# Kernel optimization log

Measured on AMD Instinct MI355X. Metric: run time of the kernel, lower is better.

The kernel has to match this reference:

```python
import jax, jax.numpy as jnp
import numpy as np

N_NODES = 50000
EPS = 1e-16


def seg_softmax(att, seg, n):
    # att: [E, H], softmax over edges sharing the same destination (seg)
    m = jax.ops.segment_max(att, seg, num_segments=n)
    m = jnp.where(jnp.isfinite(m), m, 0.0)
    e = jnp.exp(att - m[seg])
    s = jax.ops.segment_sum(e, seg, num_segments=n)
    return e / (s[seg] + EPS)


def gat_layer(x, W, b, a_l, a_r, row, col, n, nhead, out_feats, alpha, act):
    h = (x @ W).reshape(-1, nhead, out_feats)           # [N, H, F]
    h = jnp.nan_to_num(h)
    h_l = jnp.sum(a_l * h, axis=-1)                     # [N, H]
    h_r = jnp.sum(a_r * h, axis=-1)                     # [N, H]
    e = h_l[row] + h_r[col]                             # [E, H]
    e = jax.nn.leaky_relu(e, negative_slope=alpha)
    att = seg_softmax(e, row, n)                        # softmax per destination node
    # sparse multi-head aggregation: out[i] = sum_{e: row[e]=i} att[e] * h[col[e]]
    msg = att[:, :, None] * h[col]                      # [E, H, F]
    out = jax.ops.segment_sum(msg, row, num_segments=n) # [N, H, F]
    out = out.reshape(n, nhead * out_feats) + b
    if act:
        out = jax.nn.relu(out)
    return out


def setup_inputs() -> dict:
    key = jax.random.key(0)
    ks = jax.random.split(key, 10)
    N, E = N_NODES, 800000
    x = jax.random.normal(ks[0], (N, 256), dtype=jnp.float32)
    row = jax.random.randint(ks[1], (E,), 0, N)
    col = jax.random.randint(ks[2], (E,), 0, N)
    g = 1.414  # xavier-like scale handled via normal * small std
    W1 = jax.random.normal(ks[3], (256, 128), dtype=jnp.float32) * (g / np.sqrt(256 + 128))
    b1 = jnp.zeros((128,), dtype=jnp.float32)
    al1 = jax.random.normal(ks[4], (1, 4, 32), dtype=jnp.float32) * 0.1
    ar1 = jax.random.normal(ks[5], (1, 4, 32), dtype=jnp.float32) * 0.1
    W2 = jax.random.normal(ks[6], (128, 64), dtype=jnp.float32) * (g / np.sqrt(128 + 64))
    b2 = jnp.zeros((64,), dtype=jnp.float32)
    al2 = jax.random.normal(ks[7], (1, 1, 64), dtype=jnp.float32) * 0.1
    ar2 = jax.random.normal(ks[8], (1, 1, 64), dtype=jnp.float32) * 0.1
    return {"x": x, "row": row, "col": col, "W1": W1, "b1": b1, "al1": al1,
            "ar1": ar1, "W2": W2, "b2": b2, "al2": al2, "ar2": ar2}


def reference(x, row, col, W1, b1, al1, ar1, W2, b2, al2, ar2):
    n = N_NODES
    h = gat_layer(x, W1, b1, al1, ar1, row, col, n, nhead=4, out_feats=32, alpha=0.2, act=True)
    out = gat_layer(h, W2, b2, al2, ar2, row, col, n, nhead=1, out_feats=64, alpha=0.2, act=False)
    return out
```

## Files before the change

kernel.cpp:

```cpp
#include <hip/hip_runtime.h>
#include <hip/hip_bf16.h>
#include <hip/hip_fp16.h>
#include <math.h>

#define ALPHA 0.2f
#define LOG2E 1.44269504088896f
#define CAP 8192

typedef _Float16 half8 __attribute__((ext_vector_type(8)));
typedef float f32x4 __attribute__((ext_vector_type(4)));

__global__ __launch_bounds__(256) void setup_kernel(
    int* __restrict__ gcursor,
    const float* __restrict__ W1, _Float16* __restrict__ W1t,
    const float* __restrict__ W2, _Float16* __restrict__ W2t) {
    const int blk = blockIdx.x, tid = threadIdx.x;
    if (blk == 0) {
        gcursor[tid] = 0;
    } else if (blk <= 128) {
        int i = (blk - 1) * 256 + tid;
        int k = i >> 7, c = i & 127;
        W1t[c * 256 + k] = (_Float16)W1[i];
    } else {
        int j = (blk - 129) * 256 + tid;
        int k = j >> 6, c = j & 63;
        W2t[c * 128 + k] = (_Float16)W2[j];
    }
}

__global__ __launch_bounds__(256) void part_kernel(const int* __restrict__ row,
                                                   const int* __restrict__ col,
                                                   int* __restrict__ gcursor,
                                                   unsigned* __restrict__ tmp, int E) {
    __shared__ int h[256];
    __shared__ int rsv[256];
    const int tid = threadIdx.x;
    const int base = blockIdx.x * 4096;
    h[tid] = 0;
    __syncthreads();
#pragma unroll
    for (int k = 0; k < 16; ++k) {
        int i = base + k * 256 + tid;
        if (i < E) atomicAdd(&h[row[i] >> 8], 1);
    }
    __syncthreads();
    if (h[tid]) rsv[tid] = atomicAdd(&gcursor[tid], h[tid]);
    __syncthreads();
    h[tid] = 0;
    __syncthreads();
#pragma unroll
    for (int k = 0; k < 16; ++k) {
        int i = base + k * 256 + tid;
        if (i < E) {
            int r = row[i];
            int b = r >> 8;
            int loc = atomicAdd(&h[b], 1);
            tmp[(size_t)b * CAP + rsv[b] + loc] = ((unsigned)r << 16) | (unsigned)col[i];
        }
    }
}

__global__ __launch_bounds__(256) void bucket_kernel(const unsigned* __restrict__ tmp,
                                                     const int* __restrict__ gcursor,
                                                     unsigned* __restrict__ startcnt,
                                                     unsigned short* __restrict__ csr_col,
                                                     int N) {
    __shared__ int h[256];
    __shared__ int rs[256];
    __shared__ int wtot[4];
    const int k = blockIdx.x, tid = threadIdx.x;
    const int lane = tid & 63, wid = tid >> 6;
    const int base = k * CAP;
    const int count = gcursor[k];
    h[tid] = 0;
    __syncthreads();
    for (int p = tid; p < count; p += 256) atomicAdd(&h[(tmp[base + p] >> 16) & 255], 1);
    __syncthreads();
    int v = h[tid];
    int sc = v;
#pragma unroll
    for (int d = 1; d < 64; d <<= 1) {
        int u = __shfl_up(sc, d);
        if (lane >= d) sc += u;
    }
    if (lane == 63) wtot[wid] = sc;
    __syncthreads();
    int add = 0;
    for (int w = 0; w < wid; ++w) add += wtot[w];
    rs[tid] = sc - v + add + base;
    __syncthreads();
    int gr = k * 256 + tid;
    if (gr < N) startcnt[gr] = ((unsigned)rs[tid] << 11) | (unsigned)v;
    h[tid] = 0;
    __syncthreads();
    for (int p = tid; p < count; p += 256) {
        unsigned t = tmp[base + p];
        int rl = (t >> 16) & 255;
        int loc = atomicAdd(&h[rl], 1);
        csr_col[rs[rl] + loc] = (unsigned short)(t & 0xFFFF);
    }
}

__global__ __launch_bounds__(256) void gemm1_mfma(
    const float* __restrict__ x, const _Float16* __restrict__ Wt,
    const float* __restrict__ al, const float* __restrict__ ar,
    _Float16* __restrict__ h, float* __restrict__ hl, float* __restrict__ hr, int N)
{
    __shared__ _Float16 xs[32 * 256];
    const int tid = threadIdx.x;
    const int lane = tid & 63, wc = tid >> 6;
    const int row0 = blockIdx.x * 32;
    const int col0 = wc * 32;

#pragma unroll
    for (int it = 0; it < 8; ++it) {
        int i = it * 256 + tid;
        int r = i >> 6, c4 = i & 63;
        int gr = row0 + r;
        float4 v = {0.f, 0.f, 0.f, 0.f};
        if (gr < N) v = *(const float4*)(x + (size_t)gr * 256 + c4 * 4);
        union { _Float16 p[4]; uint2 u; } pk;
        pk.p[0] = (_Float16)v.x; pk.p[1] = (_Float16)v.y;
        pk.p[2] = (_Float16)v.z; pk.p[3] = (_Float16)v.w;
        int byte = r * 512 + c4 * 8;
        byte ^= (r & 7) << 4;
        *reinterpret_cast<uint2*>(reinterpret_cast<char*>(xs) + byte) = pk.u;
    }

    const _Float16* wbase = Wt + (size_t)(col0 + (lane & 15)) * 256 + (lane >> 4) * 8;

    __syncthreads();

    f32x4 acc[2][2] = {};
    half8 bf0[2], bf1[2], af0[2], af1[2];

    auto loadB = [&](int s, half8* dst) {
        dst[0] = *(const half8*)(wbase + s * 32);
        dst[1] = *(const half8*)(wbase + 16 * 256 + s * 32);
    };
    auto loadA = [&](int s, half8* dst) {
#pragma unroll
        for (int m = 0; m < 2; ++m) {
            int r = m * 16 + (lane & 15);
            int byte = r * 512 + s * 64 + (lane >> 4) * 16;
            byte ^= (r & 7) << 4;
            dst[m] = *reinterpret_cast<const half8*>(
                reinterpret_cast<const char*>(xs) + byte);
        }
    };
    auto domfma = [&](half8* a, half8* bvec) {
#pragma unroll
        for (int m = 0; m < 2; ++m)
#pragma unroll
            for (int n = 0; n < 2; ++n)
                acc[m][n] = __builtin_amdgcn_mfma_f32_16x16x32_f16(
                    a[m], bvec[n], acc[m][n], 0, 0, 0);
    };

    loadB(0, bf0); loadA(0, af0);
#pragma unroll
    for (int s = 0; s < 8; s += 2) {
        if (s + 1 < 8) { loadB(s + 1, bf1); loadA(s + 1, af1); }
        domfma(af0, bf0);
        if (s + 2 < 8) { loadB(s + 2, bf0); loadA(s + 2, af0); }
        if (s + 1 < 8) domfma(af1, bf1);
    }

#pragma unroll
    for (int m = 0; m < 2; ++m) {
        int grow_base = row0 + m * 16 + (lane >> 4) * 4;
#pragma unroll
        for (int n = 0; n < 2; ++n) {
            int gcol = col0 + n * 16 + (lane & 15);
#pragma unroll
            for (int reg = 0; reg < 4; ++reg) {
                int grow = grow_base + reg;
                if (grow < N) h[(size_t)grow * 128 + gcol] = (_Float16)acc[m][n][reg];
            }
        }
    }

    const float al0 = al[col0 + (lane & 15)],      ar0 = ar[col0 + (lane & 15)];
    const float al1 = al[col0 + 16 + (lane & 15)], ar1 = ar[col0 + 16 + (lane & 15)];
#pragma unroll
    for (int m = 0; m < 2; ++m) {
#pragma unroll
        for (int reg = 0; reg < 4; ++reg) {
            float l = al0 * acc[m][0][reg] + al1 * acc[m][1][reg];
            float r = ar0 * acc[m][0][reg] + ar1 * acc[m][1][reg];
#pragma unroll
            for (int msk = 1; msk < 16; msk <<= 1) {
                l += __shfl_xor(l, msk);
                r += __shfl_xor(r, msk);
            }
            int grow = row0 + m * 16 + (lane >> 4) * 4 + reg;
            if ((lane & 15) == 0 && grow < N) {
                hl[grow * 4 + wc] = l * LOG2E;
                hr[grow * 4 + wc] = r * LOG2E;
            }
        }
    }
}

__global__ __launch_bounds__(256) void gemm2_mfma(
    const _Float16* __restrict__ xin, const _Float16* __restrict__ Wt,
    const float* __restrict__ al, const float* __restrict__ ar,
    _Float16* __restrict__ h, float* __restrict__ hl, float* __restrict__ hr, int N)
{
    __shared__ _Float16 xs[32 * 128];
    __shared__ float plds[32][4], prds[32][4];
    const int tid = threadIdx.x;
    const int lane = tid & 63, wc = tid >> 6;
    const int row0 = blockIdx.x * 32;
    const int col0 = wc * 16;

#pragma unroll
    for (int it = 0; it < 2; ++it) {
        int i = it * 256 + tid;
        int r = i >> 4, c16 = i & 15;
        int gr = row0 + r;
        uint4 v = {0, 0, 0, 0};
        if (gr < N) v = *(const uint4*)(xin + (size_t)gr * 128 + c16 * 8);
        int byte = r * 256 + c16 * 16;
        byte ^= (r & 7) << 4;
        *reinterpret_cast<uint4*>(reinterpret_cast<char*>(xs) + byte) = v;
    }

    const _Float16* wbase = Wt + (size_t)(col0 + (lane & 15)) * 128 + (lane >> 4) * 8;

    __syncthreads();

    f32x4 acc[2] = {};
    half8 bf0, bf1, af0[2], af1[2];

    auto loadA = [&](int s, half8* dst) {
#pragma unroll
        for (int m = 0; m < 2; ++m) {
            int r = m * 16 + (lane & 15);
            int byte = r * 256 + s * 64 + (lane >> 4) * 16;
            byte ^= (r & 7) << 4;
            dst[m] = *reinterpret_cast<const half8*>(
                reinterpret_cast<const char*>(xs) + byte);
        }
    };

    bf0 = *(const half8*)(wbase); loadA(0, af0);
#pragma unroll
    for (int s = 0; s < 4; s += 2) {
        if (s + 1 < 4) { bf1 = *(const half8*)(wbase + (s + 1) * 32); loadA(s + 1, af1); }
#pragma unroll
        for (int m = 0; m < 2; ++m)
            acc[m] = __builtin_amdgcn_mfma_f32_16x16x32_f16(af0[m], bf0, acc[m], 0, 0, 0);
        if (s + 2 < 4) { bf0 = *(const half8*)(wbase + (s + 2) * 32); loadA(s + 2, af0); }
        if (s + 1 < 4)
#pragma unroll
            for (int m = 0; m < 2; ++m)
                acc[m] = __builtin_amdgcn_mfma_f32_16x16x32_f16(af1[m], bf1, acc[m], 0, 0, 0);
    }

#pragma unroll
    for (int m = 0; m < 2; ++m) {
        int grow_base = row0 + m * 16 + (lane >> 4) * 4;
        int gcol = col0 + (lane & 15);
#pragma unroll
        for (int reg = 0; reg < 4; ++reg) {
            int grow = grow_base + reg;
            if (grow < N) h[(size_t)grow * 64 + gcol] = (_Float16)acc[m][reg];
        }
    }

    const float alv = al[col0 + (lane & 15)], arv = ar[col0 + (lane & 15)];
#pragma unroll
    for (int m = 0; m < 2; ++m) {
#pragma unroll
        for (int reg = 0; reg < 4; ++reg) {
            float l = alv * acc[m][reg];
            float r = arv * acc[m][reg];
#pragma unroll
            for (int msk = 1; msk < 16; msk <<= 1) {
                l += __shfl_xor(l, msk);
                r += __shfl_xor(r, msk);
            }
            int ri = m * 16 + (lane >> 4) * 4 + reg;
            if ((lane & 15) == 0) { plds[ri][wc] = l; prds[ri][wc] = r; }
        }
    }
    __syncthreads();
    if (tid < 32) {
        int grow = row0 + tid;
        if (grow < N) {
            float l = plds[tid][0] + plds[tid][1] + plds[tid][2] + plds[tid][3];
            float r = prds[tid][0] + prds[tid][1] + prds[tid][2] + prds[tid][3];
            hl[grow] = l * LOG2E;
            hr[grow] = r * LOG2E;
        }
    }
}

__global__ __launch_bounds__(256) void agg1_kernel(
    const unsigned* __restrict__ startcnt, const unsigned short* __restrict__ csr_col,
    const float* __restrict__ hls, const float* __restrict__ hrs,
    const _Float16* __restrict__ h, const float* __restrict__ b,
    _Float16* __restrict__ out, int N)
{
    const int i = blockIdx.x * 4 + (threadIdx.x >> 6);
    if (i >= N) return;
    const int lane = threadIdx.x & 63;
    const int q = lane >> 4;
    const int fl = lane & 15;
    const int head = fl >> 2;
    const unsigned pk = startcnt[i];
    const int s = (int)(pk >> 11), e = s + (int)(pk & 2047);
    const float hlv = hls[i * 4 + head];

    float acc[8] = {};
    float den = 0.f;

    int p0 = s + q;
    bool v0 = p0 < e;
    int cc0 = v0 ? (int)csr_col[p0] : 0;
    float hr0 = hrs[cc0 * 4 + head];
    uint4 g0 = *(const uint4*)(h + (size_t)cc0 * 128 + 8 * fl);

#pragma unroll 2
    for (int pb = s; pb < e; pb += 4) {
        int p1 = pb + 4 + q;
        bool v1 = p1 < e;
        int cc1 = v1 ? (int)csr_col[p1] : 0;
        float hr1v = hrs[cc1 * 4 + head];
        uint4 g1 = *(const uint4*)(h + (size_t)cc1 * 128 + 8 * fl);

        float sc = hlv + hr0;
        sc = sc > 0.f ? sc : ALPHA * sc;
        float w = exp2f(sc);
        w = v0 ? w : 0.f;
        den += w;
        union { uint4 u; _Float16 q8[8]; } hv; hv.u = g0;
#pragma unroll
        for (int k = 0; k < 8; ++k) acc[k] = fmaf(w, (float)hv.q8[k], acc[k]);

        v0 = v1; cc0 = cc1; hr0 = hr1v; g0 = g1;
    }

    den += __shfl_xor(den, 16); den += __shfl_xor(den, 32);
#pragma unroll
    for (int k = 0; k < 8; ++k) {
        acc[k] += __shfl_xor(acc[k], 16);
        acc[k] += __shfl_xor(acc[k], 32);
    }

    if (lane < 16) {
        float r = 1.f / (den + 1e-16f);
        const float* bp = b + 8 * fl;
        union { uint4 u; _Float16 q8[8]; } ov;
#pragma unroll
        for (int k = 0; k < 8; ++k) {
            float o = acc[k] * r + bp[k];
            o = o > 0.f ? o : 0.f;
            ov.q8[k] = (_Float16)o;
        }
        *reinterpret_cast<uint4*>(out + (size_t)i * 128 + 8 * fl) = ov.u;
    }
}

__global__ __launch_bounds__(256) void agg2_kernel(
    const unsigned* __restrict__ startcnt, const unsigned short* __restrict__ csr_col,
    const float* __restrict__ hls, const float* __restrict__ hrs,
    const _Float16* __restrict__ h, const float* __restrict__ b,
    float* __restrict__ out, int N)
{
    const int i = blockIdx.x * 4 + (threadIdx.x >> 6);
    if (i >= N) return;
    const int lane = threadIdx.x & 63;
    const int q = lane >> 4;
    const int fl = lane & 15;
    const unsigned pk = startcnt[i];
    const int s = (int)(pk >> 11), e = s + (int)(pk & 2047);
    const float hlv = hls[i];

    float acc[4] = {};
    float den = 0.f;

    int p0 = s + q;
    bool v0 = p0 < e;
    int cc0 = v0 ? (int)csr_col[p0] : 0;
    float hr0 = hrs[cc0];
    uint2 g0 = *(const uint2*)(h + (size_t)cc0 * 64 + 4 * fl);

#pragma unroll 2
    for (int pb = s; pb < e; pb += 4) {
        int p1 = pb + 4 + q;
        bool v1 = p1 < e;
        int cc1 = v1 ? (int)csr_col[p1] : 0;
        float hr1v = hrs[cc1];
        uint2 g1 = *(const uint2*)(h + (size_t)cc1 * 64 + 4 * fl);

        float sc = hlv + hr0;
        sc = sc > 0.f ? sc : ALPHA * sc;
        float w = exp2f(sc);
        w = v0 ? w : 0.f;
        den += w;
        union { uint2 u; _Float16 q4[4]; } hv; hv.u = g0;
#pragma unroll
        for (int k = 0; k < 4; ++k) acc[k] = fmaf(w, (float)hv.q4[k], acc[k]);

        v0 = v1; cc0 = cc1; hr0 = hr1v; g0 = g1;
    }

    den += __shfl_xor(den, 16); den += __shfl_xor(den, 32);
#pragma unroll
    for (int k = 0; k < 4; ++k) {
        acc[k] += __shfl_xor(acc[k], 16);
        acc[k] += __shfl_xor(acc[k], 32);
    }

    if (lane < 16) {
        float r = 1.f / (den + 1e-16f);
        float4 bv = *(const float4*)(b + 4 * fl);
        float4 ov;
        ov.x = acc[0] * r + bv.x;
        ov.y = acc[1] * r + bv.y;
        ov.z = acc[2] * r + bv.z;
        ov.w = acc[3] * r + bv.w;
        *reinterpret_cast<float4*>(out + (size_t)i * 64 + 4 * fl) = ov;
    }
}

extern "C" void kernel_launch(void* const* d_in, const int* in_sizes, int n_in,
                              void* d_out, int out_size, void* d_ws, size_t ws_size,
                              hipStream_t stream)
{
    const float* x   = (const float*)d_in[0];
    const int*   row = (const int*)d_in[1];
    const int*   col = (const int*)d_in[2];
    const float* W1  = (const float*)d_in[3];
    const float* b1  = (const float*)d_in[4];
    const float* al1 = (const float*)d_in[5];
    const float* ar1 = (const float*)d_in[6];
    const float* W2  = (const float*)d_in[7];
    const float* b2  = (const float*)d_in[8];
    const float* al2 = (const float*)d_in[9];
    const float* ar2 = (const float*)d_in[10];
    const int N = in_sizes[0] / 256;
    const int E = in_sizes[1];
    const int nbuck = (N + 255) >> 8;
    float* out = (float*)d_out;

    size_t off_b = 0;
    auto alloc = [&](size_t bytes) -> void* {
        void* p = (char*)d_ws + off_b;
        off_b += (bytes + 255) & ~(size_t)255;
        return p;
    };
    int*            gcursor  = (int*)alloc((size_t)256 * 4);
    unsigned*       startcnt = (unsigned*)alloc((size_t)N * 4);
    unsigned*       tmp      = (unsigned*)alloc((size_t)nbuck * CAP * 4);
    unsigned short* csr_col  = (unsigned short*)alloc((size_t)nbuck * CAP * 2 + 32);
    _Float16*       W1t      = (_Float16*)alloc((size_t)128 * 256 * 2);
    _Float16*       W2t      = (_Float16*)alloc((size_t)64 * 128 * 2);
    _Float16*       h1       = (_Float16*)alloc((size_t)N * 128 * 2);
    float*          hl1      = (float*)alloc((size_t)N * 4 * 4);
    float*          hr1      = (float*)alloc((size_t)N * 4 * 4);
    _Float16*       out1h    = (_Float16*)alloc((size_t)N * 128 * 2);
    _Float16*       h2       = (_Float16*)alloc((size_t)N * 64 * 2);
    float*          hl2      = (float*)alloc((size_t)N * 4);
    float*          hr2      = (float*)alloc((size_t)N * 4);
    (void)ws_size; (void)n_in; (void)out_size;

    const int eblocks = (E + 4095) / 4096;

    setup_kernel<<<161, 256, 0, stream>>>(gcursor, W1, W1t, W2, W2t);
    part_kernel<<<eblocks, 256, 0, stream>>>(row, col, gcursor, tmp, E);
    bucket_kernel<<<nbuck, 256, 0, stream>>>(tmp, gcursor, startcnt, csr_col, N);

    gemm1_mfma<<<(N + 31) / 32, 256, 0, stream>>>(x, W1t, al1, ar1, h1, hl1, hr1, N);
    agg1_kernel<<<(N + 3) / 4, 256, 0, stream>>>(startcnt, csr_col, hl1, hr1, h1, b1, out1h, N);

    gemm2_mfma<<<(N + 31) / 32, 256, 0, stream>>>(out1h, W2t, al2, ar2, h2, hl2, hr2, N);
    agg2_kernel<<<(N + 3) / 4, 256, 0, stream>>>(startcnt, csr_col, hl2, hr2, h2, b2, out, N);
}
```

Measured before the change: 136.5 us.

## Split aggregation kernels into per-feature-slice launches for L2 locality

Aggregation now processes one 32-feature slice (one head in layer 1, half the features in layer 2) per block group. Block index selects the slice first, so all nodes are swept once per slice. Each lane gathers 4 bytes instead of 16 or 8. The intent is to shrink the gathered working set per sweep so neighbour rows stay in L2/MALL. The cost is re-reading CSR indices, startcnt and hr values once per slice, plus narrower, less efficient gather loads.

Measured after the change: 216.4 us. +58.5%, slower.

```diff
diff --git a/kernel.cpp b/kernel.cpp
--- a/kernel.cpp
+++ b/kernel.cpp
@@ -301,65 +301,60 @@
     const unsigned* __restrict__ startcnt, const unsigned short* __restrict__ csr_col,
     const float* __restrict__ hls, const float* __restrict__ hrs,
     const _Float16* __restrict__ h, const float* __restrict__ b,
-    _Float16* __restrict__ out, int N)
+    _Float16* __restrict__ out, int N, int nodeblocks)
 {
-    const int i = blockIdx.x * 4 + (threadIdx.x >> 6);
+    const int sl = blockIdx.x / nodeblocks;
+    const int nb = blockIdx.x - sl * nodeblocks;
+    const int i = nb * 4 + (threadIdx.x >> 6);
     if (i >= N) return;
     const int lane = threadIdx.x & 63;
     const int q = lane >> 4;
     const int fl = lane & 15;
-    const int head = fl >> 2;
     const unsigned pk = startcnt[i];
     const int s = (int)(pk >> 11), e = s + (int)(pk & 2047);
-    const float hlv = hls[i * 4 + head];
-
-    float acc[8] = {};
-    float den = 0.f;
+    const float hlv = hls[i * 4 + sl];
+    const _Float16* hsl = h + sl * 32 + 2 * fl;
+
+    float acc0 = 0.f, acc1 = 0.f, den = 0.f;
 
     int p0 = s + q;
     bool v0 = p0 < e;
     int cc0 = v0 ? (int)csr_col[p0] : 0;
-    float hr0 = hrs[cc0 * 4 + head];
-    uint4 g0 = *(const uint4*)(h + (size_t)cc0 * 128 + 8 * fl);
+    float hr0 = hrs[cc0 * 4 + sl];
+    unsigned g0 = *(const unsigned*)(hsl + (size_t)cc0 * 128);
 
 #pragma unroll 2
     for (int pb = s; pb < e; pb += 4) {
         int p1 = pb + 4 + q;
         bool v1 = p1 < e;
         int cc1 = v1 ? (int)csr_col[p1] : 0;
-        float hr1v = hrs[cc1 * 4 + head];
-        uint4 g1 = *(const uint4*)(h + (size_t)cc1 * 128 + 8 * fl);
+        float hr1v = hrs[cc1 * 4 + sl];
+        unsigned g1 = *(const unsigned*)(hsl + (size_t)cc1 * 128);
 
         float sc = hlv + hr0;
         sc = sc > 0.f ? sc : ALPHA * sc;
         float w = exp2f(sc);
         w = v0 ? w : 0.f;
         den += w;
-        union { uint4 u; _Float16 q8[8]; } hv; hv.u = g0;
-#pragma unroll
-        for (int k = 0; k < 8; ++k) acc[k] = fmaf(w, (float)hv.q8[k], acc[k]);
+        union { unsigned u; _Float16 q2[2]; } hv; hv.u = g0;
+        acc0 = fmaf(w, (float)hv.q2[0], acc0);
+        acc1 = fmaf(w, (float)hv.q2[1], acc1);
 
         v0 = v1; cc0 = cc1; hr0 = hr1v; g0 = g1;
     }
 
-    den += __shfl_xor(den, 16); den += __shfl_xor(den, 32);
-#pragma unroll
-    for (int k = 0; k < 8; ++k) {
-        acc[k] += __shfl_xor(acc[k], 16);
-        acc[k] += __shfl_xor(acc[k], 32);
-    }
+    den  += __shfl_xor(den, 16);  den  += __shfl_xor(den, 32);
+    acc0 += __shfl_xor(acc0, 16); acc0 += __shfl_xor(acc0, 32);
+    acc1 += __shfl_xor(acc1, 16); acc1 += __shfl_xor(acc1, 32);
 
     if (lane < 16) {
         float r = 1.f / (den + 1e-16f);
-        const float* bp = b + 8 * fl;
-        union { uint4 u; _Float16 q8[8]; } ov;
-#pragma unroll
-        for (int k = 0; k < 8; ++k) {
-            float o = acc[k] * r + bp[k];
-            o = o > 0.f ? o : 0.f;
-            ov.q8[k] = (_Float16)o;
-        }
-        *reinterpret_cast<uint4*>(out + (size_t)i * 128 + 8 * fl) = ov.u;
+        float2 bv = *(const float2*)(b + sl * 32 + 2 * fl);
+        float o0 = acc0 * r + bv.x; o0 = o0 > 0.f ? o0 : 0.f;
+        float o1 = acc1 * r + bv.y; o1 = o1 > 0.f ? o1 : 0.f;
+        union { unsigned u; _Float16 q2[2]; } ov;
+        ov.q2[0] = (_Float16)o0; ov.q2[1] = (_Float16)o1;
+        *reinterpret_cast<unsigned*>(out + (size_t)i * 128 + sl * 32 + 2 * fl) = ov.u;
     }
 }
 
@@ -367,9 +362,11 @@
     const unsigned* __restrict__ startcnt, const unsigned short* __restrict__ csr_col,
     const float* __restrict__ hls, const float* __restrict__ hrs,
     const _Float16* __restrict__ h, const float* __restrict__ b,
-    float* __restrict__ out, int N)
+    float* __restrict__ out, int N, int nodeblocks)
 {
-    const int i = blockIdx.x * 4 + (threadIdx.x >> 6);
+    const int sl = blockIdx.x / nodeblocks;
+    const int nb = blockIdx.x - sl * nodeblocks;
+    const int i = nb * 4 + (threadIdx.x >> 6);
     if (i >= N) return;
     const int lane = threadIdx.x & 63;
     const int q = lane >> 4;
@@ -377,15 +374,15 @@
     const unsigned pk = startcnt[i];
     const int s = (int)(pk >> 11), e = s + (int)(pk & 2047);
     const float hlv = hls[i];
-
-    float acc[4] = {};
-    float den = 0.f;
+    const _Float16* hsl = h + sl * 32 + 2 * fl;
+
+    float acc0 = 0.f, acc1 = 0.f, den = 0.f;
 
     int p0 = s + q;
     bool v0 = p0 < e;
     int cc0 = v0 ? (int)csr_col[p0] : 0;
     float hr0 = hrs[cc0];
-    uint2 g0 = *(const uint2*)(h + (size_t)cc0 * 64 + 4 * fl);
+    unsigned g0 = *(const unsigned*)(hsl + (size_t)cc0 * 64);
 
 #pragma unroll 2
     for (int pb = s; pb < e; pb += 4) {
@@ -393,36 +390,29 @@
         bool v1 = p1 < e;
         int cc1 = v1 ? (int)csr_col[p1] : 0;
         float hr1v = hrs[cc1];
-        uint2 g1 = *(const uint2*)(h + (size_t)cc1 * 64 + 4 * fl);
+        unsigned g1 = *(const unsigned*)(hsl + (size_t)cc1 * 64);
 
         float sc = hlv + hr0;
         sc = sc > 0.f ? sc : ALPHA * sc;
         float w = exp2f(sc);
         w = v0 ? w : 0.f;
         den += w;
-        union { uint2 u; _Float16 q4[4]; } hv; hv.u = g0;
-#pragma unroll
-        for (int k = 0; k < 4; ++k) acc[k] = fmaf(w, (float)hv.q4[k], acc[k]);
+        union { unsigned u; _Float16 q2[2]; } hv; hv.u = g0;
+        acc0 = fmaf(w, (float)hv.q2[0], acc0);
+        acc1 = fmaf(w, (float)hv.q2[1], acc1);
 
         v0 = v1; cc0 = cc1; hr0 = hr1v; g0 = g1;
     }
 
-    den += __shfl_xor(den, 16); den += __shfl_xor(den, 32);
-#pragma unroll
-    for (int k = 0; k < 4; ++k) {
-        acc[k] += __shfl_xor(acc[k], 16);
-        acc[k] += __shfl_xor(acc[k], 32);
-    }
+    den  += __shfl_xor(den, 16);  den  += __shfl_xor(den, 32);
+    acc0 += __shfl_xor(acc0, 16); acc0 += __shfl_xor(acc0, 32);
+    acc1 += __shfl_xor(acc1, 16); acc1 += __shfl_xor(acc1, 32);
 
     if (lane < 16) {
         float r = 1.f / (den + 1e-16f);
-        float4 bv = *(const float4*)(b + 4 * fl);
-        float4 ov;
-        ov.x = acc[0] * r + bv.x;
-        ov.y = acc[1] * r + bv.y;
-        ov.z = acc[2] * r + bv.z;
-        ov.w = acc[3] * r + bv.w;
-        *reinterpret_cast<float4*>(out + (size_t)i * 64 + 4 * fl) = ov;
+        float2 bv = *(const float2*)(b + sl * 32 + 2 * fl);
+        float2 ov = {acc0 * r + bv.x, acc1 * r + bv.y};
+        *(float2*)(out + (size_t)i * 64 + sl * 32 + 2 * fl) = ov;
     }
 }
 
@@ -468,14 +458,17 @@
     (void)ws_size; (void)n_in; (void)out_size;
 
     const int eblocks = (E + 4095) / 4096;
+    const int nodeblocks = (N + 3) / 4;
 
     setup_kernel<<<161, 256, 0, stream>>>(gcursor, W1, W1t, W2, W2t);
     part_kernel<<<eblocks, 256, 0, stream>>>(row, col, gcursor, tmp, E);
     bucket_kernel<<<nbuck, 256, 0, stream>>>(tmp, gcursor, startcnt, csr_col, N);
 
     gemm1_mfma<<<(N + 31) / 32, 256, 0, stream>>>(x, W1t, al1, ar1, h1, hl1, hr1, N);
-    agg1_kernel<<<(N + 3) / 4, 256, 0, stream>>>(startcnt, csr_col, hl1, hr1, h1, b1, out1h, N);
+    agg1_kernel<<<nodeblocks * 4, 256, 0, stream>>>(startcnt, csr_col, hl1, hr1, h1, b1,
+                                                    out1h, N, nodeblocks);
 
     gemm2_mfma<<<(N + 31) / 32, 256, 0, stream>>>(out1h, W2t, al2, ar2, h2, hl2, hr2, N);
-    agg2_kernel<<<(N + 3) / 4, 256, 0, stream>>>(startcnt, csr_col, hl2, hr2, h2, b2, out, N);
-}
+    agg2_kernel<<<nodeblocks * 2, 256, 0, stream>>>(startcnt, csr_col, hl2, hr2, h2, b2,
+                                                    out, N, nodeblocks);
+}
```

## Co-schedule GEMM1 tiles with partition and bucket kernels via block-index dispatch

Applied to the files above, without the earlier changes.

Merges the edge-partitioning and bucketing kernels with halves of the first-layer GEMM into two combined launches, where the block index selects whether a block runs graph preprocessing or a GEMM tile. This lets the independent GEMM work overlap the latency-bound, atomic-heavy CSR construction and removes one kernel launch. In exchange, every block reserves the larger 16KB shared-memory footprint and register pressure is set by the heavier GEMM path, which may reduce occupancy for the partition and bucket blocks.

After: 121.5 us. -11.0%, faster.

```diff
diff --git a/kernel.cpp b/kernel.cpp
--- a/kernel.cpp
+++ b/kernel.cpp
@@ -28,14 +28,16 @@
     }
 }
 
-__global__ __launch_bounds__(256) void part_kernel(const int* __restrict__ row,
-                                                   const int* __restrict__ col,
-                                                   int* __restrict__ gcursor,
-                                                   unsigned* __restrict__ tmp, int E) {
-    __shared__ int h[256];
-    __shared__ int rsv[256];
+
+__device__ __forceinline__ void part_body(char* smem, int blk,
+                                          const int* __restrict__ row,
+                                          const int* __restrict__ col,
+                                          int* __restrict__ gcursor,
+                                          unsigned* __restrict__ tmp, int E) {
+    int* h = (int*)smem;
+    int* rsv = h + 256;
     const int tid = threadIdx.x;
-    const int base = blockIdx.x * 4096;
+    const int base = blk * 4096;
     h[tid] = 0;
     __syncthreads();
 #pragma unroll
@@ -60,15 +62,15 @@
     }
 }
 
-__global__ __launch_bounds__(256) void bucket_kernel(const unsigned* __restrict__ tmp,
-                                                     const int* __restrict__ gcursor,
-                                                     unsigned* __restrict__ startcnt,
-                                                     unsigned short* __restrict__ csr_col,
-                                                     int N) {
-    __shared__ int h[256];
-    __shared__ int rs[256];
-    __shared__ int wtot[4];
-    const int k = blockIdx.x, tid = threadIdx.x;
+__device__ __forceinline__ void bucket_body(char* smem, int k,
+                                            const unsigned* __restrict__ tmp,
+                                            const int* __restrict__ gcursor,
+                                            unsigned* __restrict__ startcnt,
+                                            unsigned short* __restrict__ csr_col, int N) {
+    int* h = (int*)smem;
+    int* rs = h + 256;
+    int* wtot = rs + 256;
+    const int tid = threadIdx.x;
     const int lane = tid & 63, wid = tid >> 6;
     const int base = k * CAP;
     const int count = gcursor[k];
@@ -101,15 +103,18 @@
     }
 }
 
-__global__ __launch_bounds__(256) void gemm1_mfma(
-    const float* __restrict__ x, const _Float16* __restrict__ Wt,
-    const float* __restrict__ al, const float* __restrict__ ar,
-    _Float16* __restrict__ h, float* __restrict__ hl, float* __restrict__ hr, int N)
-{
-    __shared__ _Float16 xs[32 * 256];
+__device__ __forceinline__ void gemm1_body(char* smem, int tile,
+                                           const float* __restrict__ x,
+                                           const _Float16* __restrict__ Wt,
+                                           const float* __restrict__ al,
+                                           const float* __restrict__ ar,
+                                           _Float16* __restrict__ h,
+                                           float* __restrict__ hl,
+                                           float* __restrict__ hr, int N) {
+    _Float16* xs = (_Float16*)smem;
     const int tid = threadIdx.x;
     const int lane = tid & 63, wc = tid >> 6;
-    const int row0 = blockIdx.x * 32;
+    const int row0 = tile * 32;
     const int col0 = wc * 32;
 
 #pragma unroll
@@ -124,7 +129,7 @@
         pk.p[2] = (_Float16)v.z; pk.p[3] = (_Float16)v.w;
         int byte = r * 512 + c4 * 8;
         byte ^= (r & 7) << 4;
-        *reinterpret_cast<uint2*>(reinterpret_cast<char*>(xs) + byte) = pk.u;
+        *reinterpret_cast<uint2*>(smem + byte) = pk.u;
     }
 
     const _Float16* wbase = Wt + (size_t)(col0 + (lane & 15)) * 256 + (lane >> 4) * 8;
@@ -144,8 +149,7 @@
             int r = m * 16 + (lane & 15);
             int byte = r * 512 + s * 64 + (lane >> 4) * 16;
             byte ^= (r & 7) << 4;
-            dst[m] = *reinterpret_cast<const half8*>(
-                reinterpret_cast<const char*>(xs) + byte);
+            dst[m] = *reinterpret_cast<const half8*>(smem + byte);
         }
     };
     auto domfma = [&](half8* a, half8* bvec) {
@@ -200,6 +204,37 @@
             }
         }
     }
+}
+
+__global__ __launch_bounds__(256) void ka_kernel(
+    const int* __restrict__ row, const int* __restrict__ col,
+    int* __restrict__ gcursor, unsigned* __restrict__ tmp, int E, int eblocks,
+    const float* __restrict__ x, const _Float16* __restrict__ W1t,
+    const float* __restrict__ al, const float* __restrict__ ar,
+    _Float16* __restrict__ h, float* __restrict__ hl, float* __restrict__ hr,
+    int N, int tile0)
+{
+    __shared__ __align__(16) char smem[16384];
+    if (blockIdx.x < (unsigned)eblocks)
+        part_body(smem, blockIdx.x, row, col, gcursor, tmp, E);
+    else
+        gemm1_body(smem, tile0 + blockIdx.x - eblocks, x, W1t, al, ar, h, hl, hr, N);
+}
+
+__global__ __launch_bounds__(256) void kb_kernel(
+    const unsigned* __restrict__ tmp, const int* __restrict__ gcursor,
+    unsigned* __restrict__ startcnt, unsigned short* __restrict__ csr_col,
+    int nbuck,
+    const float* __restrict__ x, const _Float16* __restrict__ W1t,
+    const float* __restrict__ al, const float* __restrict__ ar,
+    _Float16* __restrict__ h, float* __restrict__ hl, float* __restrict__ hr,
+    int N, int tile0)
+{
+    __shared__ __align__(16) char smem[16384];
+    if (blockIdx.x < (unsigned)nbuck)
+        bucket_body(smem, blockIdx.x, tmp, gcursor, startcnt, csr_col, N);
+    else
+        gemm1_body(smem, tile0 + blockIdx.x - nbuck, x, W1t, al, ar, h, hl, hr, N);
 }
 
 __global__ __launch_bounds__(256) void gemm2_mfma(
@@ -468,12 +503,16 @@
     (void)ws_size; (void)n_in; (void)out_size;
 
     const int eblocks = (E + 4095) / 4096;
+    const int tiles = (N + 31) / 32;
+    const int tilesA = (tiles + 1) / 2;
+    const int tilesB = tiles - tilesA;
 
     setup_kernel<<<161, 256, 0, stream>>>(gcursor, W1, W1t, W2, W2t);
-    part_kernel<<<eblocks, 256, 0, stream>>>(row, col, gcursor, tmp, E);
-    bucket_kernel<<<nbuck, 256, 0, stream>>>(tmp, gcursor, startcnt, csr_col, N);
-
-    gemm1_mfma<<<(N + 31) / 32, 256, 0, stream>>>(x, W1t, al1, ar1, h1, hl1, hr1, N);
+    ka_kernel<<<eblocks + tilesA, 256, 0, stream>>>(row, col, gcursor, tmp, E, eblocks,
+                                                    x, W1t, al1, ar1, h1, hl1, hr1, N, 0);
+    kb_kernel<<<nbuck + tilesB, 256, 0, stream>>>(tmp, gcursor, startcnt, csr_col, nbuck,
+                                                  x, W1t, al1, ar1, h1, hl1, hr1, N, tilesA);
+
     agg1_kernel<<<(N + 3) / 4, 256, 0, stream>>>(startcnt, csr_col, hl1, hr1, h1, b1, out1h, N);
 
     gemm2_mfma<<<(N + 31) / 32, 256, 0, stream>>>(out1h, W2t, al2, ar2, h2, hl2, hr2, N);
```
